# Optimization experiments

Measured on AMD Instinct MI355X. Metric: run time of the kernel, lower is better.

Reference implementation:

```python
import jax, jax.numpy as jnp
import numpy as np

INPUT_SIZE = 64
RESERVOIR_SIZE = 2048
SPECTRAL_RADIUS = 0.9
SPARSITY = 0.1
WARMUP = 100
LEAKING_RATE = 0.01
T = 8192


def _make_weights(seed=0):
    rng = np.random.default_rng(seed)
    Win = (rng.random((RESERVOIR_SIZE, INPUT_SIZE)) - 0.5).astype(np.float32)
    Wh = (rng.random((RESERVOIR_SIZE, RESERVOIR_SIZE)) - 0.5).astype(np.float32)
    # scale to spectral radius, then apply sparsity mask (same order as the torch module)
    eig = np.linalg.eigvals(Wh.astype(np.float64))
    Wh = Wh * np.float32(SPECTRAL_RADIUS / np.max(np.abs(eig)))
    mask = (rng.random((RESERVOIR_SIZE, RESERVOIR_SIZE)) < SPARSITY).astype(np.float32)
    Wh = Wh * mask
    return jnp.asarray(Win), jnp.asarray(Wh)


def setup_inputs() -> dict:
    key = jax.random.key(0)
    x = jax.random.normal(key, (T, INPUT_SIZE), dtype=jnp.float32)
    Win, Wh = _make_weights()
    return {"x": x, "Win": Win, "Wh": Wh}


def reference(x, Win, Wh):
    lr = jnp.float32(LEAKING_RATE)

    def step(h, xt):
        h_new = jnp.tanh(Win @ xt + Wh @ h)
        h = (1.0 - lr) * h + lr * h_new
        return h, jnp.concatenate([h, xt])  # extended state [R + I]

    h0 = jnp.zeros((RESERVOIR_SIZE,), dtype=x.dtype)
    _, H_all = jax.lax.scan(step, h0, x)  # [T, R + I]
    return H_all[WARMUP:]                 # [T - warmup, R + I]
```

## Files before the change

### kernel.cpp

```cpp
#include <hip/hip_runtime.h>
#include <hip/hip_fp16.h>
#include <math.h>


#define NWG        128
#define ROWS_PER_WG 16
#define T_STEPS    8192
#define WARMUP     100
#define RSIZE      2048
#define ISIZE      64
#define OUTCOLS    2112
#define MAXREP     8
#define REP_STRIDE_W 16384
#define CAPT       24

typedef int i32x4 __attribute__((ext_vector_type(4)));

#define REP24(F) \
  F(0) F(1) F(2) F(3) F(4) F(5) F(6) F(7) \
  F(8) F(9) F(10) F(11) F(12) F(13) F(14) F(15) \
  F(16) F(17) F(18) F(19) F(20) F(21) F(22) F(23)

#define REP12(F) \
  F(0) F(1) F(2) F(3) F(4) F(5) F(6) F(7) F(8) F(9) F(10) F(11)

#define PAIRS12(F) \
  F(0,0,1) F(1,2,3) F(2,4,5) F(3,6,7) F(4,8,9) F(5,10,11) \
  F(6,12,13) F(7,14,15) F(8,16,17) F(9,18,19) F(10,20,21) F(11,22,23)

#define DECLV(I) float v##I = 0.0f;
#define DECLO(I) unsigned op##I = 0u;
#define SETV(I)  v##I = sv[l * CAPT + (I)];
#define SETO(I)  op##I = (unsigned)si[l * CAPT + 2 * (I)] | ((unsigned)si[l * CAPT + 2 * (I) + 1] << 16);
#define PINV(I)  asm volatile("" : "+v"(v##I));
#define PINO(I)  asm volatile("" : "+v"(op##I));
#define MAC2(P, A, B) \
  if ((A) < cm) { f0 = fmaf(v##A, *(const float*)(hsb + (op##P & 0xFFFFu)), f0); } \
  if ((B) < cm) { f1 = fmaf(v##B, *(const float*)(hsb + (op##P >> 16)),     f1); }

static __device__ __forceinline__ float h16_to_f32(unsigned short u) {
    __half_raw hr; hr.x = u;
    return __half2float(__half(hr));
}
static __device__ __forceinline__ unsigned short f32_to_h16(float f) {
    __half_raw hr = __half_raw(__float2half_rn(f));
    return hr.x;
}

__global__ __launch_bounds__(256) void init_ws_kernel(unsigned* rep0, int nrep) {
    int t = blockIdx.x * blockDim.x + threadIdx.x;
    if (t < nrep * RSIZE) {
        int rep = t >> 11;
        int idx = t & (RSIZE - 1);
        unsigned* b = rep0 + rep * REP_STRIDE_W;
        b[idx]         = 0u;
        b[RSIZE + idx] = 0xFFFF0000u;
    }
}

__global__ __launch_bounds__(256) void xcopy_kernel(const float* __restrict__ x,
                                                    float* __restrict__ out) {
    int t = blockIdx.x * blockDim.x + threadIdx.x;
    if (t >= (T_STEPS - WARMUP) * ISIZE) return;
    int rowo = t >> 6;
    int j    = t & 63;
    out[(size_t)rowo * OUTCOLS + RSIZE + j] = x[(size_t)(rowo + WARMUP) * ISIZE + j];
}

__global__ __launch_bounds__(256, 1) void esn_scan_kernel(
    const float* __restrict__ x,
    const float* __restrict__ Win,
    const float* __restrict__ Wh,
    float* __restrict__ out,
    unsigned* rep0,
    int nrep, int repmask)
{
    __shared__ __align__(16) float hs[RSIZE];
    __shared__ float part[64];
    __shared__ float sv[64 * CAPT];
    __shared__ unsigned short si[64 * CAPT];

    const int tid = threadIdx.x;
    const int wg  = blockIdx.x;
    const int w   = tid >> 6;
    const int l   = tid & 63;
    const int r4  = l >> 2;
    const int c4  = l & 3;
    const int row = wg * ROWS_PER_WG + r4;
    const int seg = w * 512;
    const char* hsb = (const char*)hs;

    const unsigned* myrep = rep0 + (wg & repmask) * REP_STRIDE_W;

    int cnt = 0;
    REP24(DECLV)
    REP12(DECLO)
    const float* wrow = Wh + (size_t)row * RSIZE + seg;
    for (int ph = 0; ph < 4; ++ph) {
        if (w == ph) {
            for (int i = 0; i < CAPT; ++i) { sv[l * CAPT + i] = 0.0f; si[l * CAPT + i] = 0; }
            int c = 0, c2 = 0;
            #pragma unroll 8
            for (int j = 0; j < 512; j += 4) {
                const float4 t4 = *(const float4*)(wrow + j);
                #define TAKE(VAL, COMP) \
                    if ((VAL) != 0.0f) { \
                        if ((c & 3) == c4 && c2 < CAPT) { \
                            sv[l * CAPT + c2] = (VAL); \
                            si[l * CAPT + c2] = (unsigned short)((seg + j + (COMP)) * 4); \
                            ++c2; \
                        } \
                        ++c; \
                    }
                TAKE(t4.x, 0) TAKE(t4.y, 1) TAKE(t4.z, 2) TAKE(t4.w, 3)
                #undef TAKE
            }
            cnt = c2;
            REP24(SETV)
            REP12(SETO)
        }
        __syncthreads();
    }
    REP24(PINV)
    REP12(PINO)

    int cm = cnt;
    #pragma unroll
    for (int d = 1; d < 64; d <<= 1) { const int o = __shfl_xor(cm, d); cm = o > cm ? o : cm; }
    cm = __builtin_amdgcn_readfirstlane(cm);

    float wix, wiy, wiz, wiw;
    { float4 t = *(const float4*)(Win + (size_t)row * ISIZE + w * 16 + c4 * 4);
      wix = t.x; wiy = t.y; wiz = t.z; wiw = t.w; }
    asm volatile("" : "+v"(wix), "+v"(wiy), "+v"(wiz), "+v"(wiw));

    const int prow = (tid < 128) ? (tid >> 3) : (tid - 128);
    float hcur = 0.0f;

    i32x4 xi, pA, pB, qA, qB;

    for (int k = 1; k <= T_STEPS; ++k) {
        const int psel = ((k - 1) & 1) ? RSIZE : 0;
        const unsigned* pb = myrep + psel + tid * 8;
        const float* xp = x + (size_t)(k - 1) * ISIZE + w * 16 + c4 * 4;

        asm volatile(
            "global_load_dwordx4 %0, %5, off\n\t"
            "global_load_dwordx4 %1, %6, off sc0 sc1\n\t"
            "global_load_dwordx4 %2, %6, off offset:16 sc0 sc1\n\t"
            "global_load_dwordx4 %3, %6, off sc0 sc1\n\t"
            "global_load_dwordx4 %4, %6, off offset:16 sc0 sc1\n\t"
            : "=&v"(xi), "=&v"(pA), "=&v"(pB), "=&v"(qA), "=&v"(qB)
            : "v"(xp), "v"(pb)
            : "memory");

        if (k > 1 && tid < 144) {
            const float4 ps = *(const float4*)(part + prow * 4);
            float y = ps.x + ps.y + ps.z + ps.w;
            float ax = fabsf(y);
            float e  = __expf(2.0f * ax);
            float t  = 1.0f - 2.0f / (e + 1.0f);
            t = copysignf(t, y);
            hcur = 0.99f * hcur + 0.01f * t;
            if (tid < 128) {
                if ((tid & 7) < nrep) {
                    const unsigned word = ((unsigned)(k - 1) << 16) | (unsigned)f32_to_h16(hcur);
                    const int slot = psel + wg * ROWS_PER_WG + prow;
                    __hip_atomic_store(rep0 + (tid & 7) * REP_STRIDE_W + slot, word,
                                       __ATOMIC_RELAXED, __HIP_MEMORY_SCOPE_AGENT);
                }
            } else if (k - 1 >= WARMUP + 1) {
                __builtin_nontemporal_store(
                    hcur, out + (size_t)(k - 1 - (WARMUP + 1)) * OUTCOLS + wg * ROWS_PER_WG + prow);
            }
        }

        asm volatile("s_waitcnt vmcnt(2)"
                     : "+v"(xi), "+v"(pA), "+v"(pB) :: "memory");

        const unsigned expw = (unsigned)(k - 1) << 16;
        unsigned dmask = 3u;

        #define CHECK_STAGE(QA, QB) do { \
            if (dmask & 1u) { \
                const unsigned d0 = (((unsigned)(QA).x ^ expw) | ((unsigned)(QA).y ^ expw) | \
                                     ((unsigned)(QA).z ^ expw) | ((unsigned)(QA).w ^ expw)) & 0xFFFF0000u; \
                if (d0 == 0u) { \
                    float4 f; \
                    f.x = h16_to_f32((unsigned short)((QA).x & 0xFFFF)); \
                    f.y = h16_to_f32((unsigned short)((QA).y & 0xFFFF)); \
                    f.z = h16_to_f32((unsigned short)((QA).z & 0xFFFF)); \
                    f.w = h16_to_f32((unsigned short)((QA).w & 0xFFFF)); \
                    *(float4*)(hs + tid * 8) = f; \
                    dmask &= ~1u; \
                } \
            } \
            if (dmask & 2u) { \
                const unsigned d1 = (((unsigned)(QB).x ^ expw) | ((unsigned)(QB).y ^ expw) | \
                                     ((unsigned)(QB).z ^ expw) | ((unsigned)(QB).w ^ expw)) & 0xFFFF0000u; \
                if (d1 == 0u) { \
                    float4 f; \
                    f.x = h16_to_f32((unsigned short)((QB).x & 0xFFFF)); \
                    f.y = h16_to_f32((unsigned short)((QB).y & 0xFFFF)); \
                    f.z = h16_to_f32((unsigned short)((QB).z & 0xFFFF)); \
                    f.w = h16_to_f32((unsigned short)((QB).w & 0xFFFF)); \
                    *(float4*)(hs + tid * 8 + 4) = f; \
                    dmask &= ~2u; \
                } \
            } \
        } while (0)

        #define POLL_ROUND(NA, NB, OA, OB) \
            asm volatile("global_load_dwordx4 %0, %4, off sc0 sc1\n\t" \
                         "global_load_dwordx4 %1, %4, off offset:16 sc0 sc1\n\t" \
                         "s_waitcnt vmcnt(2)" \
                         : "=&v"(NA), "=&v"(NB), "+v"(OA), "+v"(OB) \
                         : "v"(pb) : "memory")

        CHECK_STAGE(pA, pB);
        while (dmask) {
            POLL_ROUND(pA, pB, qA, qB);
            CHECK_STAGE(qA, qB);
            if (!dmask) break;
            POLL_ROUND(qA, qB, pA, pB);
            CHECK_STAGE(pA, pB);
        }
        #undef POLL_ROUND
        #undef CHECK_STAGE

        float f0 = wix * __int_as_float(xi.x);
        f0 = fmaf(wiy, __int_as_float(xi.y), f0);
        f0 = fmaf(wiz, __int_as_float(xi.z), f0);
        f0 = fmaf(wiw, __int_as_float(xi.w), f0);
        float f1 = 0.0f;

        PAIRS12(MAC2)

        float p = f0 + f1;
        p += __shfl_xor(p, 1);
        p += __shfl_xor(p, 2);
        if (c4 == 0) part[r4 * 4 + w] = p;

        asm volatile("s_waitcnt vmcnt(0)" ::: "memory");
        __syncthreads();
    }

    if (tid >= 128 && tid < 144) {
        const float4 ps = *(const float4*)(part + prow * 4);
        float y = ps.x + ps.y + ps.z + ps.w;
        float ax = fabsf(y);
        float e  = __expf(2.0f * ax);
        float t  = 1.0f - 2.0f / (e + 1.0f);
        t = copysignf(t, y);
        hcur = 0.99f * hcur + 0.01f * t;
        __builtin_nontemporal_store(
            hcur, out + (size_t)(T_STEPS - (WARMUP + 1)) * OUTCOLS + wg * ROWS_PER_WG + prow);
    }
}

extern "C" void kernel_launch(void* const* d_in, const int* in_sizes, int n_in,
                              void* d_out, int out_size, void* d_ws, size_t ws_size,
                              hipStream_t stream) {
    const float* x   = (const float*)d_in[0];
    const float* Win = (const float*)d_in[1];
    const float* Wh  = (const float*)d_in[2];
    float* out = (float*)d_out;

    unsigned* rep0 = (unsigned*)d_ws;

    int nrep = MAXREP;
    while (nrep > 1 && (size_t)nrep * (REP_STRIDE_W * 4) > ws_size) nrep >>= 1;
    int repmask = nrep - 1;

    {
        int n = nrep * RSIZE;
        init_ws_kernel<<<(n + 255) / 256, 256, 0, stream>>>(rep0, nrep);
    }

    {
        int n = (T_STEPS - WARMUP) * ISIZE;
        xcopy_kernel<<<(n + 255) / 256, 256, 0, stream>>>(x, out);
    }

    esn_scan_kernel<<<NWG, 256, 0, stream>>>(x, Win, Wh, out, rep0, nrep, repmask);
}
```

Measured before the change: 20.37 ms.

## Restructure step loop: per-slot dwordx2 polling and publish right after barrier

Each lane now polls four dwordx2 slots with coalesced lane-contiguous addresses, replacing the two strided dwordx4 halves. Each slot is reissued on its own, so stale slots are re-polled without waiting for the whole set. The tanh/update and the publish of the new state to the replicas move to the end of each iteration, right after the barrier, so results go out as soon as the partial sums are ready rather than at the start of the next iteration. The input projection is computed before polling to hide it under the wait. The risk is more load instructions in flight and subtle ordering with the vmcnt counters.

```diff
diff --git a/kernel.cpp b/kernel.cpp
--- a/kernel.cpp
+++ b/kernel.cpp
@@ -15,6 +15,7 @@
 #define CAPT       24
 
 typedef int i32x4 __attribute__((ext_vector_type(4)));
+typedef int i32x2 __attribute__((ext_vector_type(2)));
 
 #define REP24(F) \
   F(0) F(1) F(2) F(3) F(4) F(5) F(6) F(7) \
@@ -76,7 +77,7 @@
     int nrep, int repmask)
 {
     __shared__ __align__(16) float hs[RSIZE];
-    __shared__ float part[64];
+    __shared__ __align__(16) float part[64];
     __shared__ float sv[64 * CAPT];
     __shared__ unsigned short si[64 * CAPT];
 
@@ -137,24 +138,69 @@
     const int prow = (tid < 128) ? (tid >> 3) : (tid - 128);
     float hcur = 0.0f;
 
-    i32x4 xi, pA, pB, qA, qB;
+    i32x4 xi;
+    i32x2 q0, q1, q2, q3;
 
     for (int k = 1; k <= T_STEPS; ++k) {
         const int psel = ((k - 1) & 1) ? RSIZE : 0;
-        const unsigned* pb = myrep + psel + tid * 8;
+        const unsigned* lp = myrep + psel + seg + 2 * l;
         const float* xp = x + (size_t)(k - 1) * ISIZE + w * 16 + c4 * 4;
 
         asm volatile(
             "global_load_dwordx4 %0, %5, off\n\t"
-            "global_load_dwordx4 %1, %6, off sc0 sc1\n\t"
-            "global_load_dwordx4 %2, %6, off offset:16 sc0 sc1\n\t"
-            "global_load_dwordx4 %3, %6, off sc0 sc1\n\t"
-            "global_load_dwordx4 %4, %6, off offset:16 sc0 sc1\n\t"
-            : "=&v"(xi), "=&v"(pA), "=&v"(pB), "=&v"(qA), "=&v"(qB)
-            : "v"(xp), "v"(pb)
+            "global_load_dwordx2 %1, %6, off sc0 sc1\n\t"
+            "global_load_dwordx2 %2, %6, off offset:512 sc0 sc1\n\t"
+            "global_load_dwordx2 %3, %6, off offset:1024 sc0 sc1\n\t"
+            "global_load_dwordx2 %4, %6, off offset:1536 sc0 sc1\n\t"
+            : "=&v"(xi), "=&v"(q0), "=&v"(q1), "=&v"(q2), "=&v"(q3)
+            : "v"(xp), "v"(lp)
             : "memory");
 
-        if (k > 1 && tid < 144) {
+        asm volatile("s_waitcnt vmcnt(4)" : "+v"(xi) :: "memory");
+        float f0 = wix * __int_as_float(xi.x);
+        f0 = fmaf(wiy, __int_as_float(xi.y), f0);
+        f0 = fmaf(wiz, __int_as_float(xi.z), f0);
+        f0 = fmaf(wiw, __int_as_float(xi.w), f0);
+        float f1 = 0.0f;
+
+        const unsigned expw = (unsigned)(k - 1) << 16;
+        unsigned m = 0xFu;
+
+        #define SLOT(S, Q, OFFSTR) \
+            asm volatile("s_waitcnt vmcnt(3)" : "+v"(Q) :: "memory"); \
+            if (m & (1u << (S))) { \
+                const unsigned a_ = (unsigned)(Q).x, b_ = (unsigned)(Q).y; \
+                if ((((a_ ^ expw) | (b_ ^ expw)) & 0xFFFF0000u) == 0u) { \
+                    float2 v_; \
+                    v_.x = h16_to_f32((unsigned short)(a_ & 0xFFFFu)); \
+                    v_.y = h16_to_f32((unsigned short)(b_ & 0xFFFFu)); \
+                    *(float2*)(hs + seg + (S) * 128 + 2 * l) = v_; \
+                    m &= ~(1u << (S)); \
+                    if (!m) break; \
+                } \
+            } \
+            asm volatile("global_load_dwordx2 %0, %1, off " OFFSTR " sc0 sc1" \
+                         : "=&v"(Q) : "v"(lp) : "memory");
+
+        for (;;) {
+            SLOT(0, q0, "")
+            SLOT(1, q1, "offset:512")
+            SLOT(2, q2, "offset:1024")
+            SLOT(3, q3, "offset:1536")
+        }
+        #undef SLOT
+
+        PAIRS12(MAC2)
+
+        float p = f0 + f1;
+        p += __shfl_xor(p, 1);
+        p += __shfl_xor(p, 2);
+        if (c4 == 0) part[r4 * 4 + w] = p;
+
+        asm volatile("s_waitcnt vmcnt(0)" ::: "memory");
+        __syncthreads();
+
+        if (tid < 144) {
             const float4 ps = *(const float4*)(part + prow * 4);
             float y = ps.x + ps.y + ps.z + ps.w;
             float ax = fabsf(y);
@@ -164,97 +210,16 @@
             hcur = 0.99f * hcur + 0.01f * t;
             if (tid < 128) {
                 if ((tid & 7) < nrep) {
-                    const unsigned word = ((unsigned)(k - 1) << 16) | (unsigned)f32_to_h16(hcur);
-                    const int slot = psel + wg * ROWS_PER_WG + prow;
+                    const unsigned word = ((unsigned)k << 16) | (unsigned)f32_to_h16(hcur);
+                    const int slot = ((k & 1) ? RSIZE : 0) + wg * ROWS_PER_WG + prow;
                     __hip_atomic_store(rep0 + (tid & 7) * REP_STRIDE_W + slot, word,
                                        __ATOMIC_RELAXED, __HIP_MEMORY_SCOPE_AGENT);
                 }
-            } else if (k - 1 >= WARMUP + 1) {
+            } else if (k >= WARMUP + 1) {
                 __builtin_nontemporal_store(
-                    hcur, out + (size_t)(k - 1 - (WARMUP + 1)) * OUTCOLS + wg * ROWS_PER_WG + prow);
+                    hcur, out + (size_t)(k - (WARMUP + 1)) * OUTCOLS + wg * ROWS_PER_WG + prow);
             }
         }
-
-        asm volatile("s_waitcnt vmcnt(2)"
-                     : "+v"(xi), "+v"(pA), "+v"(pB) :: "memory");
-
-        const unsigned expw = (unsigned)(k - 1) << 16;
-        unsigned dmask = 3u;
-
-        #define CHECK_STAGE(QA, QB) do { \
-            if (dmask & 1u) { \
-                const unsigned d0 = (((unsigned)(QA).x ^ expw) | ((unsigned)(QA).y ^ expw) | \
-                                     ((unsigned)(QA).z ^ expw) | ((unsigned)(QA).w ^ expw)) & 0xFFFF0000u; \
-                if (d0 == 0u) { \
-                    float4 f; \
-                    f.x = h16_to_f32((unsigned short)((QA).x & 0xFFFF)); \
-                    f.y = h16_to_f32((unsigned short)((QA).y & 0xFFFF)); \
-                    f.z = h16_to_f32((unsigned short)((QA).z & 0xFFFF)); \
-                    f.w = h16_to_f32((unsigned short)((QA).w & 0xFFFF)); \
-                    *(float4*)(hs + tid * 8) = f; \
-                    dmask &= ~1u; \
-                } \
-            } \
-            if (dmask & 2u) { \
-                const unsigned d1 = (((unsigned)(QB).x ^ expw) | ((unsigned)(QB).y ^ expw) | \
-                                     ((unsigned)(QB).z ^ expw) | ((unsigned)(QB).w ^ expw)) & 0xFFFF0000u; \
-                if (d1 == 0u) { \
-                    float4 f; \
-                    f.x = h16_to_f32((unsigned short)((QB).x & 0xFFFF)); \
-                    f.y = h16_to_f32((unsigned short)((QB).y & 0xFFFF)); \
-                    f.z = h16_to_f32((unsigned short)((QB).z & 0xFFFF)); \
-                    f.w = h16_to_f32((unsigned short)((QB).w & 0xFFFF)); \
-                    *(float4*)(hs + tid * 8 + 4) = f; \
-                    dmask &= ~2u; \
-                } \
-            } \
-        } while (0)
-
-        #define POLL_ROUND(NA, NB, OA, OB) \
-            asm volatile("global_load_dwordx4 %0, %4, off sc0 sc1\n\t" \
-                         "global_load_dwordx4 %1, %4, off offset:16 sc0 sc1\n\t" \
-                         "s_waitcnt vmcnt(2)" \
-                         : "=&v"(NA), "=&v"(NB), "+v"(OA), "+v"(OB) \
-                         : "v"(pb) : "memory")
-
-        CHECK_STAGE(pA, pB);
-        while (dmask) {
-            POLL_ROUND(pA, pB, qA, qB);
-            CHECK_STAGE(qA, qB);
-            if (!dmask) break;
-            POLL_ROUND(qA, qB, pA, pB);
-            CHECK_STAGE(pA, pB);
-        }
-        #undef POLL_ROUND
-        #undef CHECK_STAGE
-
-        float f0 = wix * __int_as_float(xi.x);
-        f0 = fmaf(wiy, __int_as_float(xi.y), f0);
-        f0 = fmaf(wiz, __int_as_float(xi.z), f0);
-        f0 = fmaf(wiw, __int_as_float(xi.w), f0);
-        float f1 = 0.0f;
-
-        PAIRS12(MAC2)
-
-        float p = f0 + f1;
-        p += __shfl_xor(p, 1);
-        p += __shfl_xor(p, 2);
-        if (c4 == 0) part[r4 * 4 + w] = p;
-
-        asm volatile("s_waitcnt vmcnt(0)" ::: "memory");
-        __syncthreads();
-    }
-
-    if (tid >= 128 && tid < 144) {
-        const float4 ps = *(const float4*)(part + prow * 4);
-        float y = ps.x + ps.y + ps.z + ps.w;
-        float ax = fabsf(y);
-        float e  = __expf(2.0f * ax);
-        float t  = 1.0f - 2.0f / (e + 1.0f);
-        t = copysignf(t, y);
-        hcur = 0.99f * hcur + 0.01f * t;
-        __builtin_nontemporal_store(
-            hcur, out + (size_t)(T_STEPS - (WARMUP + 1)) * OUTCOLS + wg * ROWS_PER_WG + prow);
     }
 }
 
```

Result: faster. 19.06 ms (-6.4%).
